# Performance work log

Hardware: AMD Instinct MI355X
Metric: run time of the kernel (lower is better)

The kernel has to match this reference:

```python
import jax, jax.numpy as jnp
import numpy as np

D_MODEL = 1024
N_HEADS = 16
D_K = D_MODEL // N_HEADS


def setup_inputs() -> dict:
    key = jax.random.key(0)
    ks = jax.random.split(key, 12)
    B, P = 4, 1024
    s = 1.0 / np.sqrt(D_MODEL)
    inp = {
        'query': jax.random.normal(ks[0], (B, P, D_MODEL), jnp.float32),
        'key':   jax.random.normal(ks[1], (B, P, D_MODEL), jnp.float32),
        'value': jax.random.normal(ks[2], (B, P, D_MODEL), jnp.float32),
        'Wq': jax.random.normal(ks[3], (D_MODEL, D_MODEL), jnp.float32) * s,
        'bq': jnp.zeros((D_MODEL,), jnp.float32),
        'Wk': jax.random.normal(ks[4], (D_MODEL, D_MODEL), jnp.float32) * s,
        'bk': jnp.zeros((D_MODEL,), jnp.float32),
        'Wv': jax.random.normal(ks[5], (D_MODEL, D_MODEL), jnp.float32) * s,
        'bv': jnp.zeros((D_MODEL,), jnp.float32),
        'Wo': jax.random.normal(ks[6], (D_MODEL, D_MODEL), jnp.float32) * s,
        'bo': jnp.zeros((D_MODEL,), jnp.float32),
    }
    return inp


def reference(query, key, value, Wq, bq, Wk, bk, Wv, bv, Wo, bo):
    # Linear projections (torch Linear: x @ W.T + b)
    q = query @ Wq.T + bq
    k = key @ Wk.T + bk
    v = value @ Wv.T + bv
    B, P, _ = q.shape
    KP = k.shape[-2]
    # split heads: [B, H, P, d_k]
    q = q.reshape(B, P, N_HEADS, D_K).transpose(0, 2, 1, 3)
    k = k.reshape(B, KP, N_HEADS, D_K).transpose(0, 2, 1, 3)
    v = v.reshape(B, KP, N_HEADS, D_K).transpose(0, 2, 1, 3)
    # raw scores [B, H, P, KP]
    attn_score = jnp.einsum('bhpd,bhqd->bhpq', q, k) / jnp.sqrt(jnp.float32(D_K))
    # causal mask (masked=True path)
    causal = jnp.tril(jnp.ones((P, KP), bool))
    attn_score = jnp.where(causal, attn_score, -jnp.inf)
    probs = jax.nn.softmax(attn_score, axis=-1)
    out = jnp.einsum('bhpq,bhqd->bhpd', probs, v)
    out = out.transpose(0, 2, 1, 3).reshape(B, P, D_MODEL)
    out = out @ Wo.T + bo
    return out, attn_score
```

## Files before the change

### kernel.cpp

```cpp
#include <hip/hip_runtime.h>
#include <hip/hip_bf16.h>
#include <math.h>

#define D_MODEL 1024
#define NH 16
#define DK 64
#define BATCH 4
#define SEQ 1024
#define NEG_BIG (-1.0e30f)

typedef float f32x4 __attribute__((ext_vector_type(4)));
typedef short s16x8 __attribute__((ext_vector_type(8)));

__device__ __forceinline__ void gload_lds16(const void* g, void* l) {
    __builtin_amdgcn_global_load_lds((const __attribute__((address_space(1))) void*)g,
                                     (__attribute__((address_space(3))) void*)l, 16, 0, 0);
}

__global__ __launch_bounds__(256) void cast_bf16(const float* __restrict__ src,
                                                 __hip_bfloat16* __restrict__ dst,
                                                 int n8) {
    int i = blockIdx.x * 256 + threadIdx.x;
    if (i >= n8) return;
    float4 x = ((const float4*)src)[2 * i];
    float4 y = ((const float4*)src)[2 * i + 1];
    alignas(16) __hip_bfloat16 o[8];
    o[0] = __float2bfloat16(x.x); o[1] = __float2bfloat16(x.y);
    o[2] = __float2bfloat16(x.z); o[3] = __float2bfloat16(x.w);
    o[4] = __float2bfloat16(y.x); o[5] = __float2bfloat16(y.y);
    o[6] = __float2bfloat16(y.z); o[7] = __float2bfloat16(y.w);
    ((uint4*)dst)[i] = *(const uint4*)o;
}

__global__ __launch_bounds__(256) void gemm_bf16(const __hip_bfloat16* __restrict__ A,
                                                 const __hip_bfloat16* __restrict__ Bt,
                                                 const float* __restrict__ bias,
                                                 void* __restrict__ Cout,
                                                 int M, int N, int K, int mode) {
    __shared__ __align__(16) __hip_bfloat16 As[128 * 32];
    __shared__ __align__(16) __hip_bfloat16 Bs[128 * 32];
    const int t    = threadIdx.x;
    const int lane = t & 63;
    const int w    = t >> 6;
    const int wm   = (w >> 1) * 64;
    const int wn   = (w & 1) * 64;
    const int rl   = lane & 15;
    const int g    = lane >> 4;
    const int row0 = blockIdx.y * 128;
    const int col0 = blockIdx.x * 128;

    f32x4 acc[4][4] = {};

    for (int k0 = 0; k0 < K; k0 += 32) {
#pragma unroll
        for (int i = 0; i < 2; i++) {
            int c = w * 128 + i * 64 + lane;
            int r = c >> 2, ko = (c & 3) * 8;
            gload_lds16(A  + (size_t)(row0 + r) * K + k0 + ko,
                        As + (size_t)(w * 128 + i * 64) * 8);
            gload_lds16(Bt + (size_t)(col0 + r) * K + k0 + ko,
                        Bs + (size_t)(w * 128 + i * 64) * 8);
        }
        __syncthreads();
        s16x8 af[4], bf[4];
#pragma unroll
        for (int i = 0; i < 4; i++)
            af[i] = *(const s16x8*)&As[(wm + i * 16 + rl) * 32 + g * 8];
#pragma unroll
        for (int j = 0; j < 4; j++)
            bf[j] = *(const s16x8*)&Bs[(wn + j * 16 + rl) * 32 + g * 8];
#pragma unroll
        for (int i = 0; i < 4; i++)
#pragma unroll
            for (int j = 0; j < 4; j++)
                acc[i][j] = __builtin_amdgcn_mfma_f32_16x16x32_bf16(af[i], bf[j], acc[i][j], 0, 0, 0);
        __syncthreads();
    }

    if (mode == 0) {
        float* C = (float*)Cout;
#pragma unroll
        for (int j = 0; j < 4; j++) {
            int c = col0 + wn + j * 16 + rl;
            float bv = bias[c];
#pragma unroll
            for (int i = 0; i < 4; i++) {
                int rbase = row0 + wm + i * 16 + g * 4;
#pragma unroll
                for (int r = 0; r < 4; r++)
                    C[(size_t)(rbase + r) * N + c] = acc[i][j][r] + bv;
            }
        }
    } else if (mode == 1) {
        __hip_bfloat16* C = (__hip_bfloat16*)Cout;
#pragma unroll
        for (int j = 0; j < 4; j++) {
            int c = col0 + wn + j * 16 + rl;
            float bv = bias[c];
            int h = c >> 6, d = c & 63;
#pragma unroll
            for (int i = 0; i < 4; i++) {
                int rbase = row0 + wm + i * 16 + g * 4;
#pragma unroll
                for (int r = 0; r < 4; r++) {
                    int m = rbase + r;
                    int b = m >> 10, p = m & (SEQ - 1);
                    C[(((size_t)b * NH + h) * SEQ + p) * DK + d] =
                        __float2bfloat16(acc[i][j][r] + bv);
                }
            }
        }
    } else {
        __hip_bfloat16* C = (__hip_bfloat16*)Cout;
#pragma unroll
        for (int j = 0; j < 4; j++) {
            int c = col0 + wn + j * 16 + rl;
            float bv = bias[c];
            int h = c >> 6, d = c & 63;
#pragma unroll
            for (int i = 0; i < 4; i++) {
                int rbase = row0 + wm + i * 16 + g * 4;
                int b = rbase >> 10, p = rbase & (SEQ - 1);
                alignas(8) __hip_bfloat16 o4[4];
#pragma unroll
                for (int r = 0; r < 4; r++)
                    o4[r] = __float2bfloat16(acc[i][j][r] + bv);
                *(uint2*)&C[(((size_t)b * NH + h) * DK + d) * SEQ + p] = *(const uint2*)o4;
            }
        }
    }
}

__global__ __launch_bounds__(256) void scores_mfma(const __hip_bfloat16* __restrict__ qhm,
                                                   const __hip_bfloat16* __restrict__ khm,
                                                   float* __restrict__ S) {
    const int bh  = blockIdx.z;
    const int qi0 = blockIdx.y * 128;
    const int kj0 = blockIdx.x * 128;
    float* Sout = S + (size_t)bh * SEQ * SEQ;
    const int t = threadIdx.x;

    if (kj0 > qi0) {
        float4 neg = make_float4(NEG_BIG, NEG_BIG, NEG_BIG, NEG_BIG);
#pragma unroll
        for (int i = 0; i < 16; i++) {
            int idx = t + i * 256;
            int r = idx >> 5, c4 = idx & 31;
            *(float4*)&Sout[(size_t)(qi0 + r) * SEQ + kj0 + c4 * 4] = neg;
        }
        return;
    }

    __shared__ __align__(16) __hip_bfloat16 Qs[2 * 128 * 32];
    __shared__ __align__(16) __hip_bfloat16 Ks[2 * 128 * 32];
    const __hip_bfloat16* qb = qhm + (size_t)bh * SEQ * DK;
    const __hip_bfloat16* kb = khm + (size_t)bh * SEQ * DK;
    const int lane = t & 63;
    const int w    = t >> 6;
    const int rl   = lane & 15;
    const int g    = lane >> 4;
    const int wm   = (w >> 1) * 64;
    const int wn   = (w & 1) * 64;

#pragma unroll
    for (int i = 0; i < 4; i++) {
        int c  = w * 256 + i * 64 + lane;
        int r  = (c >> 2) & 127;
        int s  = c >> 9;
        int ko = (c & 3) * 8;
        gload_lds16(qb + (size_t)(qi0 + r) * DK + s * 32 + ko,
                    Qs + (size_t)(w * 256 + i * 64) * 8);
        gload_lds16(kb + (size_t)(kj0 + r) * DK + s * 32 + ko,
                    Ks + (size_t)(w * 256 + i * 64) * 8);
    }
    __syncthreads();

    f32x4 acc[4][4] = {};
#pragma unroll
    for (int s = 0; s < 2; s++) {
        s16x8 af[4], bf[4];
#pragma unroll
        for (int i = 0; i < 4; i++)
            af[i] = *(const s16x8*)&Qs[((s * 128) + wm + i * 16 + rl) * 32 + g * 8];
#pragma unroll
        for (int j = 0; j < 4; j++)
            bf[j] = *(const s16x8*)&Ks[((s * 128) + wn + j * 16 + rl) * 32 + g * 8];
#pragma unroll
        for (int i = 0; i < 4; i++)
#pragma unroll
            for (int j = 0; j < 4; j++)
                acc[i][j] = __builtin_amdgcn_mfma_f32_16x16x32_bf16(af[i], bf[j], acc[i][j], 0, 0, 0);
    }

    const float scale = 0.125f;
#pragma unroll
    for (int i = 0; i < 4; i++) {
        int qbase = qi0 + wm + i * 16 + g * 4;
#pragma unroll
        for (int j = 0; j < 4; j++) {
            int kj = kj0 + wn + j * 16 + rl;
#pragma unroll
            for (int r = 0; r < 4; r++) {
                int qi = qbase + r;
                Sout[(size_t)qi * SEQ + kj] = (kj <= qi) ? acc[i][j][r] * scale : NEG_BIG;
            }
        }
    }
}

__global__ __launch_bounds__(256) void rowstat(const float* __restrict__ S,
                                               float2* __restrict__ stat) {
    const int wave = threadIdx.x >> 6;
    const int lane = threadIdx.x & 63;
    const int row  = blockIdx.x * 4 + wave;
    const int p    = row & (SEQ - 1);
    const float* srow = S + (size_t)row * SEQ;
    const int len = p + 1;
    const int ntile = (len + 63) >> 6;

    float e[16];
    float m = -INFINITY;
    for (int t = 0; t < ntile; t++) {
        int j = t * 64 + lane;
        float v = (j < len) ? srow[j] : -INFINITY;
        e[t] = v;
        m = fmaxf(m, v);
    }
#pragma unroll
    for (int o = 32; o > 0; o >>= 1) m = fmaxf(m, __shfl_xor(m, o, 64));

    float sum = 0.f;
    for (int t = 0; t < ntile; t++) {
        int j = t * 64 + lane;
        sum += (j < len) ? __expf(e[t] - m) : 0.f;
    }
#pragma unroll
    for (int o = 32; o > 0; o >>= 1) sum += __shfl_xor(sum, o, 64);

    if (lane == 0) stat[row] = make_float2(m, 1.0f / sum);
}

__global__ __launch_bounds__(256) void pv_mfma(const float* __restrict__ S,
                                               const float2* __restrict__ stat,
                                               const __hip_bfloat16* __restrict__ vt,
                                               __hip_bfloat16* __restrict__ ctx) {
    __shared__ __align__(16) __hip_bfloat16 Ps[128 * 136];
    __shared__ __align__(16) __hip_bfloat16 Vs[64 * 136];
    __shared__ float mrow[128], ilrow[128];
    const int t  = threadIdx.x;
    const int bh = blockIdx.y;
    const int b  = bh >> 4;
    const int h  = bh & 15;
    const int p0 = blockIdx.x * 128;
    const float* Sb = S + (size_t)bh * SEQ * SEQ + (size_t)p0 * SEQ;
    const __hip_bfloat16* vb = vt + (size_t)bh * DK * SEQ;

    if (t < 128) {
        float2 st = stat[bh * SEQ + p0 + t];
        mrow[t]  = st.x;
        ilrow[t] = st.y;
    }
    __syncthreads();

    const int lane = t & 63;
    const int w    = t >> 6;
    const int rl   = lane & 15;
    const int g    = lane >> 4;
    const int wm   = (w >> 1) * 64;
    const int wn   = (w & 1) * 32;

    f32x4 acc[4][2] = {};
    const int ntile = (p0 >> 7) + 1;
    for (int jt = 0; jt < ntile; jt++) {
        const int j0 = jt * 128;
#pragma unroll
        for (int it = 0; it < 16; it++) {
            int idx = it * 256 + t;
            int r = idx >> 5, c4 = idx & 31;
            float4 sv = *(const float4*)&Sb[(size_t)r * SEQ + j0 + c4 * 4];
            float mr = mrow[r], il = ilrow[r];
            alignas(8) __hip_bfloat16 pb[4];
            pb[0] = __float2bfloat16(__expf(sv.x - mr) * il);
            pb[1] = __float2bfloat16(__expf(sv.y - mr) * il);
            pb[2] = __float2bfloat16(__expf(sv.z - mr) * il);
            pb[3] = __float2bfloat16(__expf(sv.w - mr) * il);
            *(uint2*)&Ps[r * 136 + c4 * 4] = *(const uint2*)pb;
        }
#pragma unroll
        for (int it = 0; it < 4; it++) {
            int idx = it * 256 + t;
            int r = idx >> 4, c = idx & 15;
            uint4 vv = *(const uint4*)&vb[(size_t)r * SEQ + j0 + c * 8];
            *(uint4*)&Vs[r * 136 + c * 8] = vv;
        }
        __syncthreads();
#pragma unroll
        for (int kk = 0; kk < 4; kk++) {
            s16x8 af[4], bf[2];
#pragma unroll
            for (int i = 0; i < 4; i++)
                af[i] = *(const s16x8*)&Ps[(wm + i * 16 + rl) * 136 + kk * 32 + g * 8];
#pragma unroll
            for (int j = 0; j < 2; j++)
                bf[j] = *(const s16x8*)&Vs[(wn + j * 16 + rl) * 136 + kk * 32 + g * 8];
#pragma unroll
            for (int i = 0; i < 4; i++)
#pragma unroll
                for (int j = 0; j < 2; j++)
                    acc[i][j] = __builtin_amdgcn_mfma_f32_16x16x32_bf16(af[i], bf[j], acc[i][j], 0, 0, 0);
        }
        __syncthreads();
    }

#pragma unroll
    for (int i = 0; i < 4; i++) {
#pragma unroll
        for (int j = 0; j < 2; j++) {
            int d = wn + j * 16 + rl;
#pragma unroll
            for (int r = 0; r < 4; r++) {
                int p = p0 + wm + i * 16 + g * 4 + r;
                ctx[((size_t)(b * SEQ + p)) * D_MODEL + h * 64 + d] =
                    __float2bfloat16(acc[i][j][r]);
            }
        }
    }
}

extern "C" void kernel_launch(void* const* d_in, const int* in_sizes, int n_in,
                              void* d_out, int out_size, void* d_ws, size_t ws_size,
                              hipStream_t stream) {
    const float* query = (const float*)d_in[0];
    const float* key_  = (const float*)d_in[1];
    const float* value = (const float*)d_in[2];
    const float* Wq    = (const float*)d_in[3];
    const float* bq    = (const float*)d_in[4];
    const float* Wk    = (const float*)d_in[5];
    const float* bk    = (const float*)d_in[6];
    const float* Wv    = (const float*)d_in[7];
    const float* bv    = (const float*)d_in[8];
    const float* Wo    = (const float*)d_in[9];
    const float* bo    = (const float*)d_in[10];

    const size_t MB   = 1024 * 1024;
    const int    NTOK = BATCH * SEQ;
    char* wsb = (char*)d_ws;
    __hip_bfloat16* Xbf = (__hip_bfloat16*)wsb;
    __hip_bfloat16* Wqb = (__hip_bfloat16*)(wsb + 8  * MB);
    __hip_bfloat16* Wkb = (__hip_bfloat16*)(wsb + 10 * MB);
    __hip_bfloat16* Wvb = (__hip_bfloat16*)(wsb + 12 * MB);
    __hip_bfloat16* Wob = (__hip_bfloat16*)(wsb + 14 * MB);
    __hip_bfloat16* qhm = (__hip_bfloat16*)(wsb + 16 * MB);
    __hip_bfloat16* khm = (__hip_bfloat16*)(wsb + 24 * MB);
    __hip_bfloat16* Vtb = (__hip_bfloat16*)(wsb + 32 * MB);
    float2* stat = (float2*)(wsb + 40 * MB);

    float* out    = (float*)d_out;
    float* scores = out + (size_t)NTOK * D_MODEL;

    const int n8X = NTOK * D_MODEL / 8;
    const int n8W = D_MODEL * D_MODEL / 8;

    cast_bf16<<<n8W / 256, 256, 0, stream>>>(Wq, Wqb, n8W);
    cast_bf16<<<n8W / 256, 256, 0, stream>>>(Wk, Wkb, n8W);
    cast_bf16<<<n8W / 256, 256, 0, stream>>>(Wv, Wvb, n8W);
    cast_bf16<<<n8W / 256, 256, 0, stream>>>(Wo, Wob, n8W);

    dim3 pgrid(D_MODEL / 128, NTOK / 128);

    cast_bf16<<<n8X / 256, 256, 0, stream>>>(query, Xbf, n8X);
    gemm_bf16<<<pgrid, 256, 0, stream>>>(Xbf, Wqb, bq, qhm, NTOK, D_MODEL, D_MODEL, 1);
    cast_bf16<<<n8X / 256, 256, 0, stream>>>(key_, Xbf, n8X);
    gemm_bf16<<<pgrid, 256, 0, stream>>>(Xbf, Wkb, bk, khm, NTOK, D_MODEL, D_MODEL, 1);
    cast_bf16<<<n8X / 256, 256, 0, stream>>>(value, Xbf, n8X);
    gemm_bf16<<<pgrid, 256, 0, stream>>>(Xbf, Wvb, bv, Vtb, NTOK, D_MODEL, D_MODEL, 2);

    scores_mfma<<<dim3(SEQ / 128, SEQ / 128, BATCH * NH), 256, 0, stream>>>(qhm, khm, scores);

    rowstat<<<(BATCH * NH * SEQ) / 4, 256, 0, stream>>>(scores, stat);

    pv_mfma<<<dim3(SEQ / 128, BATCH * NH), 256, 0, stream>>>(scores, stat, Vtb, Xbf);

    gemm_bf16<<<pgrid, 256, 0, stream>>>(Xbf, Wob, bo, out, NTOK, D_MODEL, D_MODEL, 0);
}
```

Measured before the change: 589.4 us.

## Fuse row statistics into PV with online softmax and batch QKV projections

Removes the separate rowstat pass over the full score matrix by computing a running max and sum inside the PV kernel, rescaling the accumulators per tile and normalising at the end. The three Q/K/V projection GEMMs are merged into one launch with blockIdx.z selecting the projection, after the three input casts have run into separate buffers. This drops one full read of the scores matrix and raises GEMM grid occupancy. In exchange it adds shuffle reductions and shared-memory stat updates inside the PV tile loop, and the workspace grows to hold three bf16 input copies.

```diff
diff --git a/kernel.cpp b/kernel.cpp
--- a/kernel.cpp
+++ b/kernel.cpp
@@ -32,13 +32,13 @@
     ((uint4*)dst)[i] = *(const uint4*)o;
 }
 
-__global__ __launch_bounds__(256) void gemm_bf16(const __hip_bfloat16* __restrict__ A,
-                                                 const __hip_bfloat16* __restrict__ Bt,
-                                                 const float* __restrict__ bias,
-                                                 void* __restrict__ Cout,
-                                                 int M, int N, int K, int mode) {
+__device__ __forceinline__ void gemm_body(const __hip_bfloat16* __restrict__ A,
+                                          const __hip_bfloat16* __restrict__ Bt,
+                                          const float* __restrict__ bias,
+                                          void* __restrict__ Cout, int mode) {
     __shared__ __align__(16) __hip_bfloat16 As[128 * 32];
     __shared__ __align__(16) __hip_bfloat16 Bs[128 * 32];
+    const int K = D_MODEL, N = D_MODEL;
     const int t    = threadIdx.x;
     const int lane = t & 63;
     const int w    = t >> 6;
@@ -129,6 +129,27 @@
             }
         }
     }
+}
+
+__global__ __launch_bounds__(256) void gemm_bf16(const __hip_bfloat16* __restrict__ A,
+                                                 const __hip_bfloat16* __restrict__ Bt,
+                                                 const float* __restrict__ bias,
+                                                 void* __restrict__ Cout, int mode) {
+    gemm_body(A, Bt, bias, Cout, mode);
+}
+
+__global__ __launch_bounds__(256) void gemm_qkv(
+        const __hip_bfloat16* __restrict__ Xq, const __hip_bfloat16* __restrict__ Xk,
+        const __hip_bfloat16* __restrict__ Xv,
+        const __hip_bfloat16* __restrict__ Wqb, const __hip_bfloat16* __restrict__ Wkb,
+        const __hip_bfloat16* __restrict__ Wvb,
+        const float* __restrict__ bq, const float* __restrict__ bk,
+        const float* __restrict__ bv,
+        __hip_bfloat16* __restrict__ qhm, __hip_bfloat16* __restrict__ khm,
+        __hip_bfloat16* __restrict__ vtb) {
+    if (blockIdx.z == 0)      gemm_body(Xq, Wqb, bq, qhm, 1);
+    else if (blockIdx.z == 1) gemm_body(Xk, Wkb, bk, khm, 1);
+    else                      gemm_body(Xv, Wvb, bv, vtb, 2);
 }
 
 __global__ __launch_bounds__(256) void scores_mfma(const __hip_bfloat16* __restrict__ qhm,
@@ -208,45 +229,12 @@
     }
 }
 
-__global__ __launch_bounds__(256) void rowstat(const float* __restrict__ S,
-                                               float2* __restrict__ stat) {
-    const int wave = threadIdx.x >> 6;
-    const int lane = threadIdx.x & 63;
-    const int row  = blockIdx.x * 4 + wave;
-    const int p    = row & (SEQ - 1);
-    const float* srow = S + (size_t)row * SEQ;
-    const int len = p + 1;
-    const int ntile = (len + 63) >> 6;
-
-    float e[16];
-    float m = -INFINITY;
-    for (int t = 0; t < ntile; t++) {
-        int j = t * 64 + lane;
-        float v = (j < len) ? srow[j] : -INFINITY;
-        e[t] = v;
-        m = fmaxf(m, v);
-    }
-#pragma unroll
-    for (int o = 32; o > 0; o >>= 1) m = fmaxf(m, __shfl_xor(m, o, 64));
-
-    float sum = 0.f;
-    for (int t = 0; t < ntile; t++) {
-        int j = t * 64 + lane;
-        sum += (j < len) ? __expf(e[t] - m) : 0.f;
-    }
-#pragma unroll
-    for (int o = 32; o > 0; o >>= 1) sum += __shfl_xor(sum, o, 64);
-
-    if (lane == 0) stat[row] = make_float2(m, 1.0f / sum);
-}
-
 __global__ __launch_bounds__(256) void pv_mfma(const float* __restrict__ S,
-                                               const float2* __restrict__ stat,
                                                const __hip_bfloat16* __restrict__ vt,
                                                __hip_bfloat16* __restrict__ ctx) {
     __shared__ __align__(16) __hip_bfloat16 Ps[128 * 136];
     __shared__ __align__(16) __hip_bfloat16 Vs[64 * 136];
-    __shared__ float mrow[128], ilrow[128];
+    __shared__ float mrow[128], lrow[128], scl[128];
     const int t  = threadIdx.x;
     const int bh = blockIdx.y;
     const int b  = bh >> 4;
@@ -256,9 +244,8 @@
     const __hip_bfloat16* vb = vt + (size_t)bh * DK * SEQ;
 
     if (t < 128) {
-        float2 st = stat[bh * SEQ + p0 + t];
-        mrow[t]  = st.x;
-        ilrow[t] = st.y;
+        mrow[t] = -INFINITY;
+        lrow[t] = 0.f;
     }
     __syncthreads();
 
@@ -278,13 +265,31 @@
             int idx = it * 256 + t;
             int r = idx >> 5, c4 = idx & 31;
             float4 sv = *(const float4*)&Sb[(size_t)r * SEQ + j0 + c4 * 4];
-            float mr = mrow[r], il = ilrow[r];
+            float pm = fmaxf(fmaxf(sv.x, sv.y), fmaxf(sv.z, sv.w));
+#pragma unroll
+            for (int o = 16; o > 0; o >>= 1) pm = fmaxf(pm, __shfl_xor(pm, o, 64));
+            float m_old = mrow[r];
+            float m_new = fmaxf(m_old, pm);
+            float4 p;
+            p.x = __expf(sv.x - m_new);
+            p.y = __expf(sv.y - m_new);
+            p.z = __expf(sv.z - m_new);
+            p.w = __expf(sv.w - m_new);
+            float ps = (p.x + p.y) + (p.z + p.w);
+#pragma unroll
+            for (int o = 16; o > 0; o >>= 1) ps += __shfl_xor(ps, o, 64);
             alignas(8) __hip_bfloat16 pb[4];
-            pb[0] = __float2bfloat16(__expf(sv.x - mr) * il);
-            pb[1] = __float2bfloat16(__expf(sv.y - mr) * il);
-            pb[2] = __float2bfloat16(__expf(sv.z - mr) * il);
-            pb[3] = __float2bfloat16(__expf(sv.w - mr) * il);
+            pb[0] = __float2bfloat16(p.x);
+            pb[1] = __float2bfloat16(p.y);
+            pb[2] = __float2bfloat16(p.z);
+            pb[3] = __float2bfloat16(p.w);
             *(uint2*)&Ps[r * 136 + c4 * 4] = *(const uint2*)pb;
+            if ((t & 31) == 0) {
+                float f = __expf(m_old - m_new);
+                mrow[r] = m_new;
+                lrow[r] = lrow[r] * f + ps;
+                scl[r]  = f;
+            }
         }
 #pragma unroll
         for (int it = 0; it < 4; it++) {
@@ -295,6 +300,14 @@
         }
         __syncthreads();
 #pragma unroll
+        for (int i = 0; i < 4; i++)
+#pragma unroll
+            for (int r = 0; r < 4; r++) {
+                float f = scl[wm + i * 16 + g * 4 + r];
+#pragma unroll
+                for (int j = 0; j < 2; j++) acc[i][j][r] *= f;
+            }
+#pragma unroll
         for (int kk = 0; kk < 4; kk++) {
             s16x8 af[4], bf[2];
 #pragma unroll
@@ -315,13 +328,15 @@
 #pragma unroll
     for (int i = 0; i < 4; i++) {
 #pragma unroll
-        for (int j = 0; j < 2; j++) {
-            int d = wn + j * 16 + rl;
-#pragma unroll
-            for (int r = 0; r < 4; r++) {
-                int p = p0 + wm + i * 16 + g * 4 + r;
+        for (int r = 0; r < 4; r++) {
+            int pl = wm + i * 16 + g * 4 + r;
+            float il = 1.0f / lrow[pl];
+            int p = p0 + pl;
+#pragma unroll
+            for (int j = 0; j < 2; j++) {
+                int d = wn + j * 16 + rl;
                 ctx[((size_t)(b * SEQ + p)) * D_MODEL + h * 64 + d] =
-                    __float2bfloat16(acc[i][j][r]);
+                    __float2bfloat16(acc[i][j][r] * il);
             }
         }
     }
@@ -345,15 +360,17 @@
     const size_t MB   = 1024 * 1024;
     const int    NTOK = BATCH * SEQ;
     char* wsb = (char*)d_ws;
-    __hip_bfloat16* Xbf = (__hip_bfloat16*)wsb;
-    __hip_bfloat16* Wqb = (__hip_bfloat16*)(wsb + 8  * MB);
-    __hip_bfloat16* Wkb = (__hip_bfloat16*)(wsb + 10 * MB);
-    __hip_bfloat16* Wvb = (__hip_bfloat16*)(wsb + 12 * MB);
-    __hip_bfloat16* Wob = (__hip_bfloat16*)(wsb + 14 * MB);
-    __hip_bfloat16* qhm = (__hip_bfloat16*)(wsb + 16 * MB);
-    __hip_bfloat16* khm = (__hip_bfloat16*)(wsb + 24 * MB);
-    __hip_bfloat16* Vtb = (__hip_bfloat16*)(wsb + 32 * MB);
-    float2* stat = (float2*)(wsb + 40 * MB);
+    __hip_bfloat16* Xq  = (__hip_bfloat16*)wsb;
+    __hip_bfloat16* Xk  = (__hip_bfloat16*)(wsb + 8  * MB);
+    __hip_bfloat16* Xv  = (__hip_bfloat16*)(wsb + 16 * MB);
+    __hip_bfloat16* Wqb = (__hip_bfloat16*)(wsb + 24 * MB);
+    __hip_bfloat16* Wkb = (__hip_bfloat16*)(wsb + 26 * MB);
+    __hip_bfloat16* Wvb = (__hip_bfloat16*)(wsb + 28 * MB);
+    __hip_bfloat16* Wob = (__hip_bfloat16*)(wsb + 30 * MB);
+    __hip_bfloat16* qhm = (__hip_bfloat16*)(wsb + 32 * MB);
+    __hip_bfloat16* khm = (__hip_bfloat16*)(wsb + 40 * MB);
+    __hip_bfloat16* Vtb = (__hip_bfloat16*)(wsb + 48 * MB);
+    __hip_bfloat16* ctx = Xq;
 
     float* out    = (float*)d_out;
     float* scores = out + (size_t)NTOK * D_MODEL;
@@ -365,21 +382,18 @@
     cast_bf16<<<n8W / 256, 256, 0, stream>>>(Wk, Wkb, n8W);
     cast_bf16<<<n8W / 256, 256, 0, stream>>>(Wv, Wvb, n8W);
     cast_bf16<<<n8W / 256, 256, 0, stream>>>(Wo, Wob, n8W);
+    cast_bf16<<<n8X / 256, 256, 0, stream>>>(query, Xq, n8X);
+    cast_bf16<<<n8X / 256, 256, 0, stream>>>(key_, Xk, n8X);
+    cast_bf16<<<n8X / 256, 256, 0, stream>>>(value, Xv, n8X);
 
     dim3 pgrid(D_MODEL / 128, NTOK / 128);
 
-    cast_bf16<<<n8X / 256, 256, 0, stream>>>(query, Xbf, n8X);
-    gemm_bf16<<<pgrid, 256, 0, stream>>>(Xbf, Wqb, bq, qhm, NTOK, D_MODEL, D_MODEL, 1);
-    cast_bf16<<<n8X / 256, 256, 0, stream>>>(key_, Xbf, n8X);
-    gemm_bf16<<<pgrid, 256, 0, stream>>>(Xbf, Wkb, bk, khm, NTOK, D_MODEL, D_MODEL, 1);
-    cast_bf16<<<n8X / 256, 256, 0, stream>>>(value, Xbf, n8X);
-    gemm_bf16<<<pgrid, 256, 0, stream>>>(Xbf, Wvb, bv, Vtb, NTOK, D_MODEL, D_MODEL, 2);
+    gemm_qkv<<<dim3(D_MODEL / 128, NTOK / 128, 3), 256, 0, stream>>>(
+        Xq, Xk, Xv, Wqb, Wkb, Wvb, bq, bk, bv, qhm, khm, Vtb);
 
     scores_mfma<<<dim3(SEQ / 128, SEQ / 128, BATCH * NH), 256, 0, stream>>>(qhm, khm, scores);
 
-    rowstat<<<(BATCH * NH * SEQ) / 4, 256, 0, stream>>>(scores, stat);
-
-    pv_mfma<<<dim3(SEQ / 128, BATCH * NH), 256, 0, stream>>>(scores, stat, Vtb, Xbf);
-
-    gemm_bf16<<<pgrid, 256, 0, stream>>>(Xbf, Wob, bo, out, NTOK, D_MODEL, D_MODEL, 0);
-}
+    pv_mfma<<<dim3(SEQ / 128, BATCH * NH), 256, 0, stream>>>(scores, Vtb, ctx);
+
+    gemm_bf16<<<pgrid, 256, 0, stream>>>(ctx, Wob, bo, out, 0);
+}
```

Result: no change. 599.5 us (+1.7%).
